# Kernel tuning notes

Measured on AMD Instinct MI355X. Metric: run time of the kernel, lower is better.

Reference implementation:

```python
import jax, jax.numpy as jnp
import numpy as np

N = 100000   # nodes
E = 1600000  # edges (avg degree 16)
H = 128      # hidden
S = 10000    # subgraphs
G = 64       # graphs


def setup_inputs() -> dict:
    key = jax.random.key(0)
    ks = jax.random.split(key, 8)
    def w(k, shape, fan_in):
        return jax.random.normal(k, shape, dtype=jnp.float32) * (1.0 / np.sqrt(fan_in))
    return {
        "x": jnp.ones((N, 1), dtype=jnp.float32),
        "edge_index": jax.random.randint(ks[0], (2, E), 0, N, dtype=jnp.int64),
        "node_to_subgraph": jnp.sort(jax.random.randint(ks[1], (N,), 0, S, dtype=jnp.int64)),
        "subgraph_to_graph": jnp.sort(jax.random.randint(ks[2], (S,), 0, G, dtype=jnp.int64)),
        "conv1_W1": w(ks[3], (1, H), 1),
        "conv1_b1": jnp.zeros((H,), jnp.float32),
        "conv1_W2": w(ks[4], (H, H), H),
        "conv1_b2": jnp.zeros((H,), jnp.float32),
        "convs_W1": w(ks[5], (2, H, H), H),
        "convs_b1": jnp.zeros((2, H), jnp.float32),
        "convs_W2": w(ks[6], (2, H, H), H),
        "convs_b2": jnp.zeros((2, H), jnp.float32),
    }


def _gin_layer(x, src, dst, W1, b1, W2, b2):
    # GINConv, train_eps=False, eps=0: nn((1+0)*x + sum_{j in N(i)} x_j)
    agg = jax.ops.segment_sum(x[src], dst, num_segments=x.shape[0])
    h = jax.nn.relu((x + agg) @ W1 + b1)
    return jax.nn.relu(h @ W2 + b2)


def reference(x, edge_index, node_to_subgraph, subgraph_to_graph,
              conv1_W1, conv1_b1, conv1_W2, conv1_b2,
              convs_W1, convs_b1, convs_W2, convs_b2):
    src, dst = edge_index[0], edge_index[1]
    h = _gin_layer(x, src, dst, conv1_W1, conv1_b1, conv1_W2, conv1_b2)
    for i in range(convs_W1.shape[0]):  # num_layers - 1 = 2 structurally distinct layers
        h = _gin_layer(h, src, dst, convs_W1[i], convs_b1[i], convs_W2[i], convs_b2[i])
    # global_add_pool over node_to_subgraph, then subgraph_to_graph
    h = jax.ops.segment_sum(h, node_to_subgraph, num_segments=S)
    h = jax.ops.segment_sum(h, subgraph_to_graph, num_segments=G)
    return h  # [G, H]
```

## Files before the change

### kernel.cpp

```cpp
#include <hip/hip_runtime.h>

typedef unsigned int u32;
typedef unsigned short u16;
typedef __attribute__((ext_vector_type(8))) short bf16x8;
typedef __attribute__((ext_vector_type(4))) float f32x4;

#define CAP 2560
#define CHUNK 8192
#define GMT 2

__device__ __forceinline__ float bfl(u32 v){ return __uint_as_float(v << 16); }
__device__ __forceinline__ float bfh(u32 v){ return __uint_as_float(v & 0xffff0000u); }
__device__ __forceinline__ u16 f2bf(float f){
    u32 u = __float_as_uint(f);
    u += 0x7fffu + ((u >> 16) & 1u);
    return (u16)(u >> 16);
}
__device__ __forceinline__ u32 pack2(float a, float b){
    u32 ua = __float_as_uint(a); ua += 0x7fffu + ((ua >> 16) & 1u);
    u32 ub = __float_as_uint(b); ub += 0x7fffu + ((ub >> 16) & 1u);
    return (ua >> 16) | (ub & 0xffff0000u);
}


__global__ __launch_bounds__(1024) void bucket_count(const int* __restrict__ dst,
                                                     const int* __restrict__ src,
                                                     int* __restrict__ gcur,
                                                     u32* __restrict__ slots,
                                                     int NBk, int E){
    __shared__ int cnt[800];
    int t = threadIdx.x;
    int e0 = blockIdx.x * CHUNK;
    for (int i = t; i < NBk; i += 1024) cnt[i] = 0;
    __syncthreads();
    #pragma unroll
    for (int k = 0; k < CHUNK / 1024; k++){
        int e = e0 + t + k * 1024;
        if (e < E) atomicAdd(&cnt[dst[e] >> 7], 1);
    }
    __syncthreads();
    for (int i = t; i < NBk; i += 1024){
        int c = cnt[i];
        cnt[i] = c ? atomicAdd(&gcur[i], c) : 0;
    }
    __syncthreads();
    #pragma unroll
    for (int k = 0; k < CHUNK / 1024; k++){
        int e = e0 + t + k * 1024;
        if (e < E){
            int d = dst[e];
            int b = d >> 7;
            int pos = atomicAdd(&cnt[b], 1);
            if (pos < CAP) slots[b * CAP + pos] = ((u32)(d & 127) << 17) | (u32)src[e];
        }
    }
}


__global__ __launch_bounds__(512) void bucket_csr(const int* __restrict__ gcur,
                                                  u32* __restrict__ csr,
                                                  int* __restrict__ starts,
                                                  int* __restrict__ ends,
                                                  const float* __restrict__ x,
                                                  const int* __restrict__ n2s,
                                                  const int* __restrict__ s2g,
                                                  float* __restrict__ sval,
                                                  int* __restrict__ gmap, int N){
    __shared__ u32 ebuf[CAP];
    __shared__ u32 lcsr[CAP];
    __shared__ int cnt[128], excl[128], cur[128];
    __shared__ float sacc[128];
    int b = blockIdx.x, t = threadIdx.x;
    int base = b * CAP;
    int sz = gcur[b]; if (sz > CAP) sz = CAP;
    if (t < 128){ cnt[t] = 0; sacc[t] = 0.f; }
    __syncthreads();
    for (int i = t; i < sz; i += 512){
        u32 p = csr[base + i];
        ebuf[i] = p;
        atomicAdd(&cnt[p >> 17], 1);
        atomicAdd(&sacc[p >> 17], x[p & 0x1FFFFu]);
    }
    __syncthreads();
    if (t < 64){
        int c0 = cnt[2 * t], c1 = cnt[2 * t + 1];
        int tot = c0 + c1;
        int incl = tot;
        #pragma unroll
        for (int o = 1; o < 64; o <<= 1){
            int v = __shfl_up(incl, o);
            if (t >= o) incl += v;
        }
        int ex = incl - tot;
        excl[2 * t] = ex;
        excl[2 * t + 1] = ex + c0;
    }
    __syncthreads();
    if (t < 128){
        int node = b * 128 + t;
        if (node < N){
            int st = base + excl[t];
            starts[node] = st;
            ends[node] = st + cnt[t];
            sval[node] = x[node] + sacc[t];
            gmap[node] = s2g[n2s[node]];
        }
        cur[t] = excl[t];
    }
    __syncthreads();
    for (int i = t; i < sz; i += 512){
        u32 p = ebuf[i];
        int dl = p >> 17;
        int r = atomicAdd(&cur[dl], 1);
        lcsr[r] = p & 0x1FFFFu;
    }
    __syncthreads();
    if (t < 128){
        int s0 = excl[t], e0 = s0 + cnt[t];
        for (int i = s0 + 1; i < e0; i++){
            u32 key = lcsr[i];
            int j = i - 1;
            while (j >= s0 && lcsr[j] > key){ lcsr[j + 1] = lcsr[j]; j--; }
            lcsr[j + 1] = key;
        }
    }
    __syncthreads();
    for (int i = t; i < sz; i += 512) csr[base + i] = lcsr[i];
}


struct W5 { const float* p[5]; };

__global__ void pack_k(W5 w5, u16* __restrict__ wp,
                       int* __restrict__ gcur, int ngcur,
                       float* __restrict__ outz, int nout){
    int m = blockIdx.x;
    int t = threadIdx.x;
    if (m == 5){
        for (int i = t; i < ngcur; i += 256) gcur[i] = 0;
        return;
    }
    if (m == 6){
        for (int i = t; i < nout; i += 256) outz[i] = 0.f;
        return;
    }
    const float* W = w5.p[m];
    u16* dstp = wp + m * 16384;
    #pragma unroll
    for (int it = 0; it < 8; it++){
        int task = t + 256 * it;
        int n = task & 127, c = task >> 7;
        u16 tmp[8];
        #pragma unroll
        for (int j = 0; j < 8; j++) tmp[j] = f2bf(W[(c * 8 + j) * 128 + n]);
        uint4 val;
        val.x = (u32)tmp[0] | ((u32)tmp[1] << 16);
        val.y = (u32)tmp[2] | ((u32)tmp[3] << 16);
        val.z = (u32)tmp[4] | ((u32)tmp[5] << 16);
        val.w = (u32)tmp[6] | ((u32)tmp[7] << 16);
        *(uint4*)(dstp + n * 128 + ((c ^ ((n >> 3) & 15)) << 3)) = val;
    }
}


__global__ __launch_bounds__(256) void gemm1_fused(const float* __restrict__ sval,
                                                   const float* __restrict__ W1,
                                                   const float* __restrict__ b1,
                                                   const u16* __restrict__ Wp,
                                                   const float* __restrict__ bias,
                                                   u16* __restrict__ Out, int nrows){
    __shared__ float w1s[128], b1s[128];
    int t = threadIdx.x;
    if (t < 128){ w1s[t] = W1[t]; b1s[t] = b1[t]; }
    __syncthreads();

    int wave = t >> 6, lane = t & 63;
    int m = lane & 15, q = lane >> 4;
    int r0 = blockIdx.x * (64 * GMT) + wave * (16 * GMT);

    float sv[GMT];
    #pragma unroll
    for (int mt = 0; mt < GMT; mt++){
        int row = r0 + mt * 16 + m;
        if (row >= nrows) row = nrows - 1;
        sv[mt] = sval[row];
    }

    f32x4 acc[GMT][8];
    #pragma unroll
    for (int a = 0; a < GMT; a++)
        #pragma unroll
        for (int b = 0; b < 8; b++){ f32x4 z = {0.f, 0.f, 0.f, 0.f}; acc[a][b] = z; }

    #pragma unroll
    for (int kt = 0; kt < 4; kt++){
        int c = kt * 4 + q;
        int k0 = kt * 32 + q * 8;
        float wk[8], bk[8];
        #pragma unroll
        for (int j = 0; j < 8; j++){ wk[j] = w1s[k0 + j]; bk[j] = b1s[k0 + j]; }
        bf16x8 bfrag[8];
        #pragma unroll
        for (int nt = 0; nt < 8; nt++){
            int n = m * 8 + nt;
            bfrag[nt] = *(const bf16x8*)(Wp + n * 128 + ((c ^ m) << 3));
        }
        #pragma unroll
        for (int mt = 0; mt < GMT; mt++){
            bf16x8 afrag;
            #pragma unroll
            for (int j = 0; j < 8; j++){
                float v = sv[mt] * wk[j] + bk[j];
                v = v > 0.f ? v : 0.f;
                afrag[j] = (short)f2bf(v);
            }
            #pragma unroll
            for (int nt = 0; nt < 8; nt++)
                acc[mt][nt] = __builtin_amdgcn_mfma_f32_16x16x32_bf16(afrag, bfrag[nt], acc[mt][nt], 0, 0, 0);
        }
    }

    float4 bb0 = *(const float4*)(bias + m * 8);
    float4 bb1 = *(const float4*)(bias + m * 8 + 4);
    float bb[8] = {bb0.x, bb0.y, bb0.z, bb0.w, bb1.x, bb1.y, bb1.z, bb1.w};
    #pragma unroll
    for (int mt = 0; mt < GMT; mt++){
        #pragma unroll
        for (int r = 0; r < 4; r++){
            int row = r0 + mt * 16 + q * 4 + r;
            if (row < nrows){
                float v[8];
                #pragma unroll
                for (int j = 0; j < 8; j++){
                    float vv = acc[mt][j][r] + bb[j];
                    v[j] = vv > 0.f ? vv : 0.f;
                }
                uint4 o;
                o.x = pack2(v[0], v[1]);
                o.y = pack2(v[2], v[3]);
                o.z = pack2(v[4], v[5]);
                o.w = pack2(v[6], v[7]);
                *(uint4*)(Out + row * 128 + m * 8) = o;
            }
        }
    }
}


__global__ __launch_bounds__(256) void gemm2_fused(const u16* A,
                                                   const u16* __restrict__ Wp1,
                                                   const u16* __restrict__ Wp2,
                                                   const float* __restrict__ bias1,
                                                   const float* __restrict__ bias2,
                                                   u16* Out, int nrows){
    __shared__ uint4 hbuf[2048];
    u16* lds1 = (u16*)hbuf;
    int t = threadIdx.x;

    int wave = t >> 6, lane = t & 63;
    int m = lane & 15, q = lane >> 4;
    int rl0 = wave * (16 * GMT);
    int r0 = blockIdx.x * (64 * GMT) + rl0;

    f32x4 acc[GMT][8];
    #pragma unroll
    for (int a = 0; a < GMT; a++)
        #pragma unroll
        for (int b = 0; b < 8; b++){ f32x4 z = {0.f, 0.f, 0.f, 0.f}; acc[a][b] = z; }

    #pragma unroll
    for (int kt = 0; kt < 4; kt++){
        int c = kt * 4 + q;
        bf16x8 bfrag[8];
        #pragma unroll
        for (int nt = 0; nt < 8; nt++){
            int n = m * 8 + nt;
            bfrag[nt] = *(const bf16x8*)(Wp1 + n * 128 + ((c ^ m) << 3));
        }
        #pragma unroll
        for (int mt = 0; mt < GMT; mt++){
            int row = r0 + mt * 16 + m;
            if (row >= nrows) row = nrows - 1;
            bf16x8 afrag = *(const bf16x8*)(A + row * 128 + kt * 32 + q * 8);
            #pragma unroll
            for (int nt = 0; nt < 8; nt++)
                acc[mt][nt] = __builtin_amdgcn_mfma_f32_16x16x32_bf16(afrag, bfrag[nt], acc[mt][nt], 0, 0, 0);
        }
    }

    {
        float4 bb0 = *(const float4*)(bias1 + m * 8);
        float4 bb1 = *(const float4*)(bias1 + m * 8 + 4);
        float bb[8] = {bb0.x, bb0.y, bb0.z, bb0.w, bb1.x, bb1.y, bb1.z, bb1.w};
        #pragma unroll
        for (int mt = 0; mt < GMT; mt++){
            #pragma unroll
            for (int r = 0; r < 4; r++){
                int rl = rl0 + mt * 16 + q * 4 + r;
                float v[8];
                #pragma unroll
                for (int j = 0; j < 8; j++){
                    float vv = acc[mt][j][r] + bb[j];
                    v[j] = vv > 0.f ? vv : 0.f;
                }
                uint4 o;
                o.x = pack2(v[0], v[1]);
                o.y = pack2(v[2], v[3]);
                o.z = pack2(v[4], v[5]);
                o.w = pack2(v[6], v[7]);
                *(uint4*)(lds1 + rl * 128 + ((m ^ (rl & 15)) << 3)) = o;
            }
        }
    }
    __syncthreads();

    #pragma unroll
    for (int a = 0; a < GMT; a++)
        #pragma unroll
        for (int b = 0; b < 8; b++){ f32x4 z = {0.f, 0.f, 0.f, 0.f}; acc[a][b] = z; }

    #pragma unroll
    for (int kt = 0; kt < 4; kt++){
        int c = kt * 4 + q;
        bf16x8 bfrag[8];
        #pragma unroll
        for (int nt = 0; nt < 8; nt++){
            int n = m * 8 + nt;
            bfrag[nt] = *(const bf16x8*)(Wp2 + n * 128 + ((c ^ m) << 3));
        }
        #pragma unroll
        for (int mt = 0; mt < GMT; mt++){
            int rl = rl0 + mt * 16 + m;
            bf16x8 afrag = *(const bf16x8*)(lds1 + rl * 128 + (((kt * 4 + q) ^ (rl & 15)) << 3));
            #pragma unroll
            for (int nt = 0; nt < 8; nt++)
                acc[mt][nt] = __builtin_amdgcn_mfma_f32_16x16x32_bf16(afrag, bfrag[nt], acc[mt][nt], 0, 0, 0);
        }
    }

    float4 bb0 = *(const float4*)(bias2 + m * 8);
    float4 bb1 = *(const float4*)(bias2 + m * 8 + 4);
    float bb[8] = {bb0.x, bb0.y, bb0.z, bb0.w, bb1.x, bb1.y, bb1.z, bb1.w};
    #pragma unroll
    for (int mt = 0; mt < GMT; mt++){
        #pragma unroll
        for (int r = 0; r < 4; r++){
            int row = r0 + mt * 16 + q * 4 + r;
            if (row < nrows){
                float v[8];
                #pragma unroll
                for (int j = 0; j < 8; j++){
                    float vv = acc[mt][j][r] + bb[j];
                    v[j] = vv > 0.f ? vv : 0.f;
                }
                uint4 o;
                o.x = pack2(v[0], v[1]);
                o.y = pack2(v[2], v[3]);
                o.z = pack2(v[4], v[5]);
                o.w = pack2(v[6], v[7]);
                *(uint4*)(Out + row * 128 + m * 8) = o;
            }
        }
    }
}


__device__ __forceinline__ void acc8(float* a, uint4 u){
    a[0] += bfl(u.x); a[1] += bfh(u.x);
    a[2] += bfl(u.y); a[3] += bfh(u.y);
    a[4] += bfl(u.z); a[5] += bfh(u.z);
    a[6] += bfl(u.w); a[7] += bfh(u.w);
}

__global__ __launch_bounds__(256) void agg_k(const uint4* __restrict__ Hin, uint4* __restrict__ Hout,
                                             const int* __restrict__ starts, const int* __restrict__ ends,
                                             const u32* __restrict__ csr, int N){
    int gtid = blockIdx.x * 256 + threadIdx.x;
    int node = gtid >> 4;
    int c = threadIdx.x & 15;
    if (node >= N) return;

    uint4 v = Hin[node * 16 + c];
    float a[8];
    a[0] = bfl(v.x); a[1] = bfh(v.x);
    a[2] = bfl(v.y); a[3] = bfh(v.y);
    a[4] = bfl(v.z); a[5] = bfh(v.z);
    a[6] = bfl(v.w); a[7] = bfh(v.w);

    int b0 = starts[node], b1 = ends[node];
    int j = b0;
    for (; j + 4 <= b1; j += 4){
        int s0 = csr[j], s1 = csr[j + 1], s2 = csr[j + 2], s3 = csr[j + 3];
        uint4 u0 = Hin[s0 * 16 + c];
        uint4 u1 = Hin[s1 * 16 + c];
        uint4 u2 = Hin[s2 * 16 + c];
        uint4 u3 = Hin[s3 * 16 + c];
        acc8(a, u0); acc8(a, u1); acc8(a, u2); acc8(a, u3);
    }
    for (; j < b1; j++){
        int s = csr[j];
        uint4 u = Hin[s * 16 + c];
        acc8(a, u);
    }

    uint4 o;
    o.x = pack2(a[0], a[1]);
    o.y = pack2(a[2], a[3]);
    o.z = pack2(a[4], a[5]);
    o.w = pack2(a[6], a[7]);
    Hout[node * 16 + c] = o;
}


__global__ __launch_bounds__(256) void pool2_k(const u32* __restrict__ H,
                                               const int* __restrict__ gmap,
                                               float* __restrict__ out, int N){
    int c = threadIdx.x & 63;
    int seg = blockIdx.x * 4 + (threadIdx.x >> 6);
    int start = seg * 64;
    if (start >= N) return;
    int end = start + 64; if (end > N) end = N;
    int g = gmap[start];
    float a0 = 0.f, a1 = 0.f;
    for (int n = start; n < end; n++){
        int gn = gmap[n];
        if (gn != g){
            unsafeAtomicAdd(&out[g * 128 + 2 * c], a0);
            unsafeAtomicAdd(&out[g * 128 + 2 * c + 1], a1);
            a0 = 0.f; a1 = 0.f; g = gn;
        }
        u32 u = H[n * 64 + c];
        a0 += bfl(u);
        a1 += bfh(u);
    }
    unsafeAtomicAdd(&out[g * 128 + 2 * c], a0);
    unsafeAtomicAdd(&out[g * 128 + 2 * c + 1], a1);
}

extern "C" void kernel_launch(void* const* d_in, const int* in_sizes, int n_in,
                              void* d_out, int out_size, void* d_ws, size_t ws_size,
                              hipStream_t stream){
    const float* x    = (const float*)d_in[0];
    const int*   ei   = (const int*)d_in[1];
    const int*   n2s  = (const int*)d_in[2];
    const int*   s2g  = (const int*)d_in[3];
    const float* c1W1 = (const float*)d_in[4];
    const float* c1b1 = (const float*)d_in[5];
    const float* c1W2 = (const float*)d_in[6];
    const float* c1b2 = (const float*)d_in[7];
    const float* cW1  = (const float*)d_in[8];
    const float* cb1  = (const float*)d_in[9];
    const float* cW2  = (const float*)d_in[10];
    const float* cb2  = (const float*)d_in[11];
    float* out = (float*)d_out;

    int N = in_sizes[0];
    int E = in_sizes[1] / 2;
    const int* src = ei;
    const int* dst = ei + E;
    int NBk = (N + 127) / 128;

    char* w = (char*)d_ws;
    size_t off = 0;
    auto al = [&](size_t b){ size_t r = off; off += (b + 255) & ~(size_t)255; return r; };
    int*   gcur   = (int*)(w + al((size_t)NBk * 4));
    int*   starts = (int*)(w + al((size_t)N * 4));
    int*   ends   = (int*)(w + al((size_t)N * 4));
    float* sval   = (float*)(w + al((size_t)N * 4));
    int*   gmap   = (int*)(w + al((size_t)N * 4));
    u32*   csr    = (u32*)(w + al((size_t)NBk * CAP * 4));
    u16*   wp     = (u16*)(w + al((size_t)5 * 16384 * 2));
    u16*   P      = (u16*)(w + al((size_t)N * 128 * 2));
    u16*   Q      = (u16*)(w + al((size_t)N * 128 * 2));

    W5 w5;
    w5.p[0] = c1W2;
    w5.p[1] = cW1;
    w5.p[2] = cW2;
    w5.p[3] = cW1 + 16384;
    w5.p[4] = cW2 + 16384;
    pack_k<<<7, 256, 0, stream>>>(w5, wp, gcur, NBk, out, out_size);

    bucket_count<<<(E + CHUNK - 1) / CHUNK, 1024, 0, stream>>>(dst, src, gcur, csr, NBk, E);
    bucket_csr<<<NBk, 512, 0, stream>>>(gcur, csr, starts, ends, x, n2s, s2g, sval, gmap, N);

    int gG = (N + 64 * GMT - 1) / (64 * GMT);
    int gA = (N * 16 + 255) / 256;
    gemm1_fused<<<gG, 256, 0, stream>>>(sval, c1W1, c1b1, wp + 0 * 16384, c1b2, P, N);
    agg_k<<<gA, 256, 0, stream>>>((const uint4*)P, (uint4*)Q, starts, ends, csr, N);
    gemm2_fused<<<gG, 256, 0, stream>>>(Q, wp + 1 * 16384, wp + 2 * 16384, cb1, cb2, Q, N);
    agg_k<<<gA, 256, 0, stream>>>((const uint4*)Q, (uint4*)P, starts, ends, csr, N);
    gemm2_fused<<<gG, 256, 0, stream>>>(P, wp + 3 * 16384, wp + 4 * 16384, cb1 + 128, cb2 + 128, P, N);
    pool2_k<<<(N + 255) / 256, 256, 0, stream>>>((const u32*)P, gmap, out, N);
}
```

Measured before the change: 368.0 us.

## Fuse first-layer GEMM into bucket_csr and drop per-node neighbor sort

```diff
diff --git a/kernel.cpp b/kernel.cpp
--- a/kernel.cpp
+++ b/kernel.cpp
@@ -64,16 +64,19 @@
                                                   const float* __restrict__ x,
                                                   const int* __restrict__ n2s,
                                                   const int* __restrict__ s2g,
-                                                  float* __restrict__ sval,
-                                                  int* __restrict__ gmap, int N){
+                                                  int* __restrict__ gmap,
+                                                  const float* __restrict__ W1,
+                                                  const float* __restrict__ b1v,
+                                                  const u16* __restrict__ Wp,
+                                                  const float* __restrict__ bias,
+                                                  u16* __restrict__ P, int N){
     __shared__ u32 ebuf[CAP];
-    __shared__ u32 lcsr[CAP];
     __shared__ int cnt[128], excl[128], cur[128];
-    __shared__ float sacc[128];
+    __shared__ float sacc[128], svals[128], w1s[128], b1s[128];
     int b = blockIdx.x, t = threadIdx.x;
     int base = b * CAP;
     int sz = gcur[b]; if (sz > CAP) sz = CAP;
-    if (t < 128){ cnt[t] = 0; sacc[t] = 0.f; }
+    if (t < 128){ cnt[t] = 0; sacc[t] = 0.f; svals[t] = 0.f; w1s[t] = W1[t]; b1s[t] = b1v[t]; }
     __syncthreads();
     for (int i = t; i < sz; i += 512){
         u32 p = csr[base + i];
@@ -102,7 +105,7 @@
             int st = base + excl[t];
             starts[node] = st;
             ends[node] = st + cnt[t];
-            sval[node] = x[node] + sacc[t];
+            svals[t] = x[node] + sacc[t];
             gmap[node] = s2g[n2s[node]];
         }
         cur[t] = excl[t];
@@ -112,20 +115,61 @@
         u32 p = ebuf[i];
         int dl = p >> 17;
         int r = atomicAdd(&cur[dl], 1);
-        lcsr[r] = p & 0x1FFFFu;
-    }
-    __syncthreads();
-    if (t < 128){
-        int s0 = excl[t], e0 = s0 + cnt[t];
-        for (int i = s0 + 1; i < e0; i++){
-            u32 key = lcsr[i];
-            int j = i - 1;
-            while (j >= s0 && lcsr[j] > key){ lcsr[j + 1] = lcsr[j]; j--; }
-            lcsr[j + 1] = key;
-        }
-    }
-    __syncthreads();
-    for (int i = t; i < sz; i += 512) csr[base + i] = lcsr[i];
+        csr[base + r] = p & 0x1FFFFu;
+    }
+
+    int wave = t >> 6, lane = t & 63;
+    int m = lane & 15, q = lane >> 4;
+    int rl0 = wave * 16;
+    float sv = svals[rl0 + m];
+
+    f32x4 acc[8];
+    #pragma unroll
+    for (int nt = 0; nt < 8; nt++){ f32x4 z = {0.f, 0.f, 0.f, 0.f}; acc[nt] = z; }
+
+    #pragma unroll
+    for (int kt = 0; kt < 4; kt++){
+        int c = kt * 4 + q;
+        int k0 = kt * 32 + q * 8;
+        bf16x8 afrag;
+        #pragma unroll
+        for (int j = 0; j < 8; j++){
+            float v = sv * w1s[k0 + j] + b1s[k0 + j];
+            v = v > 0.f ? v : 0.f;
+            afrag[j] = (short)f2bf(v);
+        }
+        bf16x8 bfrag[8];
+        #pragma unroll
+        for (int nt = 0; nt < 8; nt++){
+            int n = m * 8 + nt;
+            bfrag[nt] = *(const bf16x8*)(Wp + n * 128 + ((c ^ m) << 3));
+        }
+        #pragma unroll
+        for (int nt = 0; nt < 8; nt++)
+            acc[nt] = __builtin_amdgcn_mfma_f32_16x16x32_bf16(afrag, bfrag[nt], acc[nt], 0, 0, 0);
+    }
+
+    float4 bb0 = *(const float4*)(bias + m * 8);
+    float4 bb1 = *(const float4*)(bias + m * 8 + 4);
+    float bb[8] = {bb0.x, bb0.y, bb0.z, bb0.w, bb1.x, bb1.y, bb1.z, bb1.w};
+    #pragma unroll
+    for (int r = 0; r < 4; r++){
+        int row = b * 128 + rl0 + q * 4 + r;
+        if (row < N){
+            float v[8];
+            #pragma unroll
+            for (int j = 0; j < 8; j++){
+                float vv = acc[j][r] + bb[j];
+                v[j] = vv > 0.f ? vv : 0.f;
+            }
+            uint4 o;
+            o.x = pack2(v[0], v[1]);
+            o.y = pack2(v[2], v[3]);
+            o.z = pack2(v[4], v[5]);
+            o.w = pack2(v[6], v[7]);
+            *(uint4*)(P + row * 128 + m * 8) = o;
+        }
+    }
 }
 
 
@@ -159,90 +203,6 @@
         val.z = (u32)tmp[4] | ((u32)tmp[5] << 16);
         val.w = (u32)tmp[6] | ((u32)tmp[7] << 16);
         *(uint4*)(dstp + n * 128 + ((c ^ ((n >> 3) & 15)) << 3)) = val;
-    }
-}
-
-
-__global__ __launch_bounds__(256) void gemm1_fused(const float* __restrict__ sval,
-                                                   const float* __restrict__ W1,
-                                                   const float* __restrict__ b1,
-                                                   const u16* __restrict__ Wp,
-                                                   const float* __restrict__ bias,
-                                                   u16* __restrict__ Out, int nrows){
-    __shared__ float w1s[128], b1s[128];
-    int t = threadIdx.x;
-    if (t < 128){ w1s[t] = W1[t]; b1s[t] = b1[t]; }
-    __syncthreads();
-
-    int wave = t >> 6, lane = t & 63;
-    int m = lane & 15, q = lane >> 4;
-    int r0 = blockIdx.x * (64 * GMT) + wave * (16 * GMT);
-
-    float sv[GMT];
-    #pragma unroll
-    for (int mt = 0; mt < GMT; mt++){
-        int row = r0 + mt * 16 + m;
-        if (row >= nrows) row = nrows - 1;
-        sv[mt] = sval[row];
-    }
-
-    f32x4 acc[GMT][8];
-    #pragma unroll
-    for (int a = 0; a < GMT; a++)
-        #pragma unroll
-        for (int b = 0; b < 8; b++){ f32x4 z = {0.f, 0.f, 0.f, 0.f}; acc[a][b] = z; }
-
-    #pragma unroll
-    for (int kt = 0; kt < 4; kt++){
-        int c = kt * 4 + q;
-        int k0 = kt * 32 + q * 8;
-        float wk[8], bk[8];
-        #pragma unroll
-        for (int j = 0; j < 8; j++){ wk[j] = w1s[k0 + j]; bk[j] = b1s[k0 + j]; }
-        bf16x8 bfrag[8];
-        #pragma unroll
-        for (int nt = 0; nt < 8; nt++){
-            int n = m * 8 + nt;
-            bfrag[nt] = *(const bf16x8*)(Wp + n * 128 + ((c ^ m) << 3));
-        }
-        #pragma unroll
-        for (int mt = 0; mt < GMT; mt++){
-            bf16x8 afrag;
-            #pragma unroll
-            for (int j = 0; j < 8; j++){
-                float v = sv[mt] * wk[j] + bk[j];
-                v = v > 0.f ? v : 0.f;
-                afrag[j] = (short)f2bf(v);
-            }
-            #pragma unroll
-            for (int nt = 0; nt < 8; nt++)
-                acc[mt][nt] = __builtin_amdgcn_mfma_f32_16x16x32_bf16(afrag, bfrag[nt], acc[mt][nt], 0, 0, 0);
-        }
-    }
-
-    float4 bb0 = *(const float4*)(bias + m * 8);
-    float4 bb1 = *(const float4*)(bias + m * 8 + 4);
-    float bb[8] = {bb0.x, bb0.y, bb0.z, bb0.w, bb1.x, bb1.y, bb1.z, bb1.w};
-    #pragma unroll
-    for (int mt = 0; mt < GMT; mt++){
-        #pragma unroll
-        for (int r = 0; r < 4; r++){
-            int row = r0 + mt * 16 + q * 4 + r;
-            if (row < nrows){
-                float v[8];
-                #pragma unroll
-                for (int j = 0; j < 8; j++){
-                    float vv = acc[mt][j][r] + bb[j];
-                    v[j] = vv > 0.f ? vv : 0.f;
-                }
-                uint4 o;
-                o.x = pack2(v[0], v[1]);
-                o.y = pack2(v[2], v[3]);
-                o.z = pack2(v[4], v[5]);
-                o.w = pack2(v[6], v[7]);
-                *(uint4*)(Out + row * 128 + m * 8) = o;
-            }
-        }
     }
 }
 
@@ -466,7 +426,6 @@
     int*   gcur   = (int*)(w + al((size_t)NBk * 4));
     int*   starts = (int*)(w + al((size_t)N * 4));
     int*   ends   = (int*)(w + al((size_t)N * 4));
-    float* sval   = (float*)(w + al((size_t)N * 4));
     int*   gmap   = (int*)(w + al((size_t)N * 4));
     u32*   csr    = (u32*)(w + al((size_t)NBk * CAP * 4));
     u16*   wp     = (u16*)(w + al((size_t)5 * 16384 * 2));
@@ -482,11 +441,11 @@
     pack_k<<<7, 256, 0, stream>>>(w5, wp, gcur, NBk, out, out_size);
 
     bucket_count<<<(E + CHUNK - 1) / CHUNK, 1024, 0, stream>>>(dst, src, gcur, csr, NBk, E);
-    bucket_csr<<<NBk, 512, 0, stream>>>(gcur, csr, starts, ends, x, n2s, s2g, sval, gmap, N);
+    bucket_csr<<<NBk, 512, 0, stream>>>(gcur, csr, starts, ends, x, n2s, s2g, gmap,
+                                        c1W1, c1b1, wp + 0 * 16384, c1b2, P, N);
 
     int gG = (N + 64 * GMT - 1) / (64 * GMT);
     int gA = (N * 16 + 255) / 256;
-    gemm1_fused<<<gG, 256, 0, stream>>>(sval, c1W1, c1b1, wp + 0 * 16384, c1b2, P, N);
     agg_k<<<gA, 256, 0, stream>>>((const uint4*)P, (uint4*)Q, starts, ends, csr, N);
     gemm2_fused<<<gG, 256, 0, stream>>>(Q, wp + 1 * 16384, wp + 2 * 16384, cb1, cb2, Q, N);
     agg_k<<<gA, 256, 0, stream>>>((const uint4*)Q, (uint4*)P, starts, ends, csr, N);
```

Measured after the change: 325.4 us. -11.6%, faster.
